# Performance work log

Measured on AMD Instinct MI355X. Metric: run time of the kernel, lower is better.

The kernel has to match this reference:

```python
import jax, jax.numpy as jnp
import numpy as np

B, X, C = 8, 256, 256  # batch, feature axis, topfreq

def setup_inputs() -> dict:
    key = jax.random.key(0)
    k1, k2, k3, k4 = jax.random.split(key, 4)
    return {
        "amplitude": jax.random.normal(k1, (B, X, C), dtype=jnp.float32),
        "phase": jax.random.normal(k2, (B, X, C), dtype=jnp.float32),
        "A": jax.random.normal(k3, (C, C), dtype=jnp.float32),
        "w_amplitude": jnp.asarray(0.5, dtype=jnp.float32),
        "w_phase": jnp.asarray(0.5, dtype=jnp.float32),
        # uniform noise for gumbel sampling; keep away from 0 to avoid -log(-log(0))
        "gumbel_u": jax.random.uniform(k4, (B, C, C, 2), dtype=jnp.float32, minval=1e-6, maxval=1.0),
    }

def reference(amplitude, phase, A, w_amplitude, w_phase, gumbel_u):
    # pairwise diffs: (b, x, c, c)
    a_diff = amplitude[..., :, None] - amplitude[..., None, :]
    p_diff = phase[..., :, None] - phase[..., None, :]
    fused = w_amplitude * a_diff + w_phase * p_diff
    # einsum 'dd,bxcd->bxcd' == multiply by diag(A) along last dim
    temp = jnp.diagonal(A) * fused
    # einsum 'bxcd,bxcd->bcd' == sum of squares over x
    dist = jnp.sum(temp * temp, axis=1)  # (b, c, c)
    exp_dist = 1.0 / (dist + 1e-10)
    eye = jnp.eye(C, dtype=exp_dist.dtype)
    off_diag = 1.0 - eye
    exp_dist = exp_dist * off_diag
    exp_max = jax.lax.stop_gradient(jnp.max(exp_dist, axis=-1, keepdims=True))
    p = exp_dist / exp_max
    p = (p * off_diag + eye) * 0.99  # (b, c, c) in (0, 0.99]
    # bernoulli via 2-class gumbel-softmax (tau=1, hard, straight-through)
    logit = jnp.log(p / (1.0 - p))
    logits = jnp.stack([logit, -logit], axis=-1)  # (b, c, c, 2)
    g = -jnp.log(-jnp.log(gumbel_u))
    y = jax.nn.softmax(logits + g, axis=-1)
    y0 = y[..., 0]
    hard0 = (y0 > y[..., 1]).astype(y.dtype)
    sample = hard0 - jax.lax.stop_gradient(y0) + y0  # straight-through
    mask = sample.mean(axis=0)  # (c, c)
    return mask
```

## Files before the change

### kernel.cpp

```cpp
#include <hip/hip_runtime.h>

#define BB 8
#define XX 256
#define CC 256
#define TC 4
#define G  8


#define STEPU(UC, ACC) {                         \
    float diff = __fsub_rn(UC, ud);              \
    float t    = __fmul_rn(dAd, diff);           \
    float sq   = __fmul_rn(t, t);                \
    ACC = __fadd_rn(ACC, sq);                    \
}

#define LOADG(BA, BP, GIDX) {                    \
    const float* _a = ampbd + (size_t)(GIDX) * G * CC; \
    const float* _p = phbd  + (size_t)(GIDX) * G * CC; \
    _Pragma("unroll")                            \
    for (int i = 0; i < G; ++i) {                \
        BA[i] = _a[(size_t)i * CC];              \
        BP[i] = _p[(size_t)i * CC];              \
    }                                            \
}

#define COMPG(BA, BP, GIDX) {                    \
    const int _xb = (GIDX) * G;                  \
    _Pragma("unroll")                            \
    for (int i = 0; i < G; ++i) {                \
        const float av = BA[i];                  \
        const float pv = BP[i];                  \
        const float ud = __fadd_rn(__fmul_rn(wa, av), __fmul_rn(wp, pv)); \
        const float4 uc = cols[_xb + i];         \
        STEPU(uc.x, acc0)                        \
        STEPU(uc.y, acc1)                        \
        STEPU(uc.z, acc2)                        \
        STEPU(uc.w, acc3)                        \
    }                                            \
}

template<int XPB>
__device__ __forceinline__ void dist_loop(
    const float* __restrict__ ampbd, const float* __restrict__ phbd,
    const float4* cols, float wa, float wp, float dAd,
    float& acc0, float& acc1, float& acc2, float& acc3)
{
    constexpr int NG = XPB / G;
    float b0A[G], b0P[G], b1A[G], b1P[G];
    LOADG(b0A, b0P, 0)
    for (int g = 0; g + 2 < NG; g += 2) {
        LOADG(b1A, b1P, g + 1)
        COMPG(b0A, b0P, g)
        LOADG(b0A, b0P, g + 2)
        COMPG(b1A, b1P, g + 1)
    }
    LOADG(b1A, b1P, NG - 1)
    COMPG(b0A, b0P, NG - 2)
    COMPG(b1A, b1P, NG - 1)
}

template<int XPB>
__device__ __forceinline__ void stage_cols(
    const float* __restrict__ amp, const float* __restrict__ ph,
    int b, int x0, int c0, float wa, float wp, float4* cols)
{
    if (threadIdx.x < XPB) {
        const int x = threadIdx.x;
        const size_t base = ((size_t)b * XX + (x0 + x)) * CC + c0;
        const float4 a4 = *(const float4*)(amp + base);
        const float4 p4 = *(const float4*)(ph  + base);
        float4 u;
        u.x = __fadd_rn(__fmul_rn(wa, a4.x), __fmul_rn(wp, p4.x));
        u.y = __fadd_rn(__fmul_rn(wa, a4.y), __fmul_rn(wp, p4.y));
        u.z = __fadd_rn(__fmul_rn(wa, a4.z), __fmul_rn(wp, p4.z));
        u.w = __fadd_rn(__fmul_rn(wa, a4.w), __fmul_rn(wp, p4.w));
        cols[x] = u;
    }
    __syncthreads();
}

__device__ __forceinline__ void epilogue(
    float dist0, float dist1, float dist2, float dist3,
    int b, int c0, int d, const float* __restrict__ gu,
    float* __restrict__ out, float (*wmax)[4])
{
    float ed[TC];
    ed[0] = (d == c0)     ? 0.0f : __fdiv_rn(1.0f, __fadd_rn(dist0, 1e-10f));
    ed[1] = (d == c0 + 1) ? 0.0f : __fdiv_rn(1.0f, __fadd_rn(dist1, 1e-10f));
    ed[2] = (d == c0 + 2) ? 0.0f : __fdiv_rn(1.0f, __fadd_rn(dist2, 1e-10f));
    ed[3] = (d == c0 + 3) ? 0.0f : __fdiv_rn(1.0f, __fadd_rn(dist3, 1e-10f));

    const int wave = threadIdx.x >> 6;
    const int lane = threadIdx.x & 63;
#pragma unroll
    for (int j = 0; j < TC; ++j) {
        float v = ed[j];
#pragma unroll
        for (int m = 1; m < 64; m <<= 1) v = fmaxf(v, __shfl_xor(v, m));
        if (lane == 0) wmax[j][wave] = v;
    }
    __syncthreads();

#pragma unroll
    for (int j = 0; j < TC; ++j) {
        const int c = c0 + j;
        float em = fmaxf(fmaxf(wmax[j][0], wmax[j][1]), fmaxf(wmax[j][2], wmax[j][3]));
        float p;
        if (d == c) {
            p = 0.99f;
        } else {
            p = __fmul_rn(__fdiv_rn(ed[j], em), 0.99f);
        }
        float logit = logf(__fdiv_rn(p, __fsub_rn(1.0f, p)));

        const float2 g2 = *(const float2*)(gu + (((size_t)b * CC + c) * CC + d) * 2);
        float g0 = -logf(-logf(g2.x));
        float g1 = -logf(-logf(g2.y));

        float a0 = __fadd_rn(logit, g0);
        float a1 = __fadd_rn(-logit, g1);
        float m  = fmaxf(a0, a1);
        float e0 = expf(__fsub_rn(a0, m));
        float e1 = expf(__fsub_rn(a1, m));
        float s  = __fadd_rn(e0, e1);
        float y0 = __fdiv_rn(e0, s);
        float y1 = __fdiv_rn(e1, s);
        if (y0 > y1) {
            atomicAdd(&out[(size_t)c * CC + d], 0.125f);
        }
    }
}


__global__ __launch_bounds__(256, 4) void k_dist(
    const float* __restrict__ amp, const float* __restrict__ ph,
    const float* __restrict__ A,   const float* __restrict__ wAp,
    const float* __restrict__ wPp, float* __restrict__ wsd)
{
    const int d    = threadIdx.x;
    const int c0   = blockIdx.x * TC;
    const int b    = blockIdx.y;
    const int half = blockIdx.z;
    const int x0   = half * (XX / 2);

    const float wa = wAp[0];
    const float wp = wPp[0];

    __shared__ float4 cols[XX / 2];
    stage_cols<XX / 2>(amp, ph, b, x0, c0, wa, wp, cols);

    const float dAd = A[(size_t)d * CC + d];
    const float* ampbd = amp + ((size_t)b * XX + x0) * CC + d;
    const float* phbd  = ph  + ((size_t)b * XX + x0) * CC + d;

    float acc0 = 0.0f, acc1 = 0.0f, acc2 = 0.0f, acc3 = 0.0f;
    dist_loop<XX / 2>(ampbd, phbd, cols, wa, wp, dAd, acc0, acc1, acc2, acc3);

    float* w = wsd + (((size_t)half * BB + b) * CC + c0) * CC + d;
    w[0 * CC] = acc0;
    w[1 * CC] = acc1;
    w[2 * CC] = acc2;
    w[3 * CC] = acc3;
}

__global__ __launch_bounds__(256, 2) void k_epi(
    const float* __restrict__ wsd, const float* __restrict__ gu,
    float* __restrict__ out)
{
    const int d  = threadIdx.x;
    const int c0 = blockIdx.x * TC;
    const int b  = blockIdx.y;

    const float* w0 = wsd + (((size_t)0 * BB + b) * CC + c0) * CC + d;
    const float* w1 = wsd + (((size_t)1 * BB + b) * CC + c0) * CC + d;
    float dist0 = __fadd_rn(w0[0 * CC], w1[0 * CC]);
    float dist1 = __fadd_rn(w0[1 * CC], w1[1 * CC]);
    float dist2 = __fadd_rn(w0[2 * CC], w1[2 * CC]);
    float dist3 = __fadd_rn(w0[3 * CC], w1[3 * CC]);

    __shared__ float wmax[TC][4];
    epilogue(dist0, dist1, dist2, dist3, b, c0, d, gu, out, wmax);
}


__global__ __launch_bounds__(256, 2) void k_fused(
    const float* __restrict__ amp, const float* __restrict__ ph,
    const float* __restrict__ A,   const float* __restrict__ wAp,
    const float* __restrict__ wPp, const float* __restrict__ gu,
    float* __restrict__ out)
{
    const int d  = threadIdx.x;
    const int c0 = blockIdx.x * TC;
    const int b  = blockIdx.y;

    const float wa = wAp[0];
    const float wp = wPp[0];

    __shared__ float4 cols[XX];
    stage_cols<XX>(amp, ph, b, 0, c0, wa, wp, cols);

    const float dAd = A[(size_t)d * CC + d];
    const float* ampbd = amp + (size_t)b * XX * CC + d;
    const float* phbd  = ph  + (size_t)b * XX * CC + d;

    float acc0 = 0.0f, acc1 = 0.0f, acc2 = 0.0f, acc3 = 0.0f;
    dist_loop<XX>(ampbd, phbd, cols, wa, wp, dAd, acc0, acc1, acc2, acc3);

    __shared__ float wmax[TC][4];
    epilogue(acc0, acc1, acc2, acc3, b, c0, d, gu, out, wmax);
}

extern "C" void kernel_launch(void* const* d_in, const int* in_sizes, int n_in,
                              void* d_out, int out_size, void* d_ws, size_t ws_size,
                              hipStream_t stream) {
    const float* amp = (const float*)d_in[0];
    const float* ph  = (const float*)d_in[1];
    const float* A   = (const float*)d_in[2];
    const float* wa  = (const float*)d_in[3];
    const float* wp  = (const float*)d_in[4];
    const float* gu  = (const float*)d_in[5];
    float* out = (float*)d_out;

    hipMemsetAsync(out, 0, (size_t)CC * CC * sizeof(float), stream);

    const size_t need = 2ull * BB * CC * CC * sizeof(float);
    if (ws_size >= need) {
        float* wsd = (float*)d_ws;
        dim3 g1(CC / TC, BB, 2);
        k_dist<<<g1, 256, 0, stream>>>(amp, ph, A, wa, wp, wsd);
        dim3 g2(CC / TC, BB);
        k_epi<<<g2, 256, 0, stream>>>(wsd, gu, out);
    } else {
        dim3 g(CC / TC, BB);
        k_fused<<<g, 256, 0, stream>>>(amp, ph, A, wa, wp, gu, out);
    }
}
```

Before: 92.00 us.

## Precompute fused u and expand squared distance as norms minus dot products

Adds a pre-pass kernel that computes u = wa*amp + wp*ph once into workspace, so the distance kernel reads one array instead of two. The per-x squared difference is rewritten as |u_c|^2 + |u_d|^2 - 2 u_c·u_d, accumulated with FMAs, and the diag(A)^2 scale is moved into the epilogue. The x reduction is split four ways instead of two, and the distance kernel's occupancy bound is raised. The expansion risks cancellation error when u_c and u_d are close, which could flip Bernoulli samples relative to the reference, and it adds a kernel launch plus extra workspace traffic.

```diff
diff --git a/kernel.cpp b/kernel.cpp
--- a/kernel.cpp
+++ b/kernel.cpp
@@ -5,6 +5,169 @@
 #define CC 256
 #define TC 4
 #define G  8
+#define SPLIT 4
+#define XH (XX / SPLIT)
+
+
+
+__device__ __forceinline__ void epilogue(
+    float dist0, float dist1, float dist2, float dist3,
+    int b, int c0, int d, const float* __restrict__ gu,
+    float* __restrict__ out, float (*wmax)[4])
+{
+    float ed[TC];
+    ed[0] = (d == c0)     ? 0.0f : __fdiv_rn(1.0f, __fadd_rn(dist0, 1e-10f));
+    ed[1] = (d == c0 + 1) ? 0.0f : __fdiv_rn(1.0f, __fadd_rn(dist1, 1e-10f));
+    ed[2] = (d == c0 + 2) ? 0.0f : __fdiv_rn(1.0f, __fadd_rn(dist2, 1e-10f));
+    ed[3] = (d == c0 + 3) ? 0.0f : __fdiv_rn(1.0f, __fadd_rn(dist3, 1e-10f));
+
+    const int wave = threadIdx.x >> 6;
+    const int lane = threadIdx.x & 63;
+#pragma unroll
+    for (int j = 0; j < TC; ++j) {
+        float v = ed[j];
+#pragma unroll
+        for (int m = 1; m < 64; m <<= 1) v = fmaxf(v, __shfl_xor(v, m));
+        if (lane == 0) wmax[j][wave] = v;
+    }
+    __syncthreads();
+
+#pragma unroll
+    for (int j = 0; j < TC; ++j) {
+        const int c = c0 + j;
+        float em = fmaxf(fmaxf(wmax[j][0], wmax[j][1]), fmaxf(wmax[j][2], wmax[j][3]));
+        float p;
+        if (d == c) {
+            p = 0.99f;
+        } else {
+            p = __fmul_rn(__fdiv_rn(ed[j], em), 0.99f);
+        }
+        float logit = logf(__fdiv_rn(p, __fsub_rn(1.0f, p)));
+
+        const float2 g2 = *(const float2*)(gu + (((size_t)b * CC + c) * CC + d) * 2);
+        float g0 = -logf(-logf(g2.x));
+        float g1 = -logf(-logf(g2.y));
+
+        float a0 = __fadd_rn(logit, g0);
+        float a1 = __fadd_rn(-logit, g1);
+        float m  = fmaxf(a0, a1);
+        float e0 = expf(__fsub_rn(a0, m));
+        float e1 = expf(__fsub_rn(a1, m));
+        float s  = __fadd_rn(e0, e1);
+        float y0 = __fdiv_rn(e0, s);
+        float y1 = __fdiv_rn(e1, s);
+        if (y0 > y1) {
+            atomicAdd(&out[(size_t)c * CC + d], 0.125f);
+        }
+    }
+}
+
+
+__global__ __launch_bounds__(256) void k_u(
+    const float* __restrict__ amp, const float* __restrict__ ph,
+    const float* __restrict__ wAp, const float* __restrict__ wPp,
+    float* __restrict__ u)
+{
+    const float wa = wAp[0], wp = wPp[0];
+    const int i = blockIdx.x * 256 + threadIdx.x;
+    const float4 a = ((const float4*)amp)[i];
+    const float4 p = ((const float4*)ph)[i];
+    float4 r;
+    r.x = __fadd_rn(__fmul_rn(wa, a.x), __fmul_rn(wp, p.x));
+    r.y = __fadd_rn(__fmul_rn(wa, a.y), __fmul_rn(wp, p.y));
+    r.z = __fadd_rn(__fmul_rn(wa, a.z), __fmul_rn(wp, p.z));
+    r.w = __fadd_rn(__fmul_rn(wa, a.w), __fmul_rn(wp, p.w));
+    ((float4*)u)[i] = r;
+}
+
+#define ULOAD(BU, GIDX) {                                  \
+    const float* _p = ud_ptr + (size_t)(GIDX) * G * CC;    \
+    _Pragma("unroll")                                      \
+    for (int i = 0; i < G; ++i) BU[i] = _p[(size_t)i * CC]; }
+
+#define UCOMP(BU, GIDX) {                                  \
+    const int _xb = (GIDX) * G;                            \
+    _Pragma("unroll")                                      \
+    for (int i = 0; i < G; ++i) {                          \
+        const float udv = BU[i];                           \
+        const float4 c4 = colsU[_xb + i];                  \
+        gacc0 = fmaf(c4.x, udv, gacc0);                    \
+        gacc1 = fmaf(c4.y, udv, gacc1);                    \
+        gacc2 = fmaf(c4.z, udv, gacc2);                    \
+        gacc3 = fmaf(c4.w, udv, gacc3);                    \
+        sacc  = fmaf(udv, udv, sacc);                      \
+    } }
+
+__global__ __launch_bounds__(256, 8) void k_dist(
+    const float* __restrict__ u,
+    float* __restrict__ wsd)
+{
+    const int d    = threadIdx.x;
+    const int c0   = blockIdx.x * TC;
+    const int b    = blockIdx.y;
+    const int x0   = blockIdx.z * XH;
+
+    __shared__ float4 colsU[XH];
+    if (threadIdx.x < XH) {
+        colsU[threadIdx.x] =
+            *(const float4*)(u + ((size_t)b * XX + x0 + threadIdx.x) * CC + c0);
+    }
+    __syncthreads();
+
+    const float* ud_ptr = u + ((size_t)b * XX + x0) * CC + d;
+
+    float gacc0 = 0.0f, gacc1 = 0.0f, gacc2 = 0.0f, gacc3 = 0.0f, sacc = 0.0f;
+
+    constexpr int NGH = XH / G;
+    float b0[G], b1[G];
+    ULOAD(b0, 0)
+    for (int g = 0; g + 2 < NGH; g += 2) {
+        ULOAD(b1, g + 1)
+        UCOMP(b0, g)
+        ULOAD(b0, g + 2)
+        UCOMP(b1, g + 1)
+    }
+    ULOAD(b1, NGH - 1)
+    UCOMP(b0, NGH - 2)
+    UCOMP(b1, NGH - 1)
+
+    __shared__ float sS[CC];
+    sS[d] = sacc;
+    __syncthreads();
+    const float sc0 = sS[c0], sc1 = sS[c0 + 1], sc2 = sS[c0 + 2], sc3 = sS[c0 + 3];
+
+    float* w = wsd + (((size_t)blockIdx.z * BB + b) * CC + c0) * CC + d;
+    w[0 * CC] = fmaf(-2.0f, gacc0, __fadd_rn(sc0, sacc));
+    w[1 * CC] = fmaf(-2.0f, gacc1, __fadd_rn(sc1, sacc));
+    w[2 * CC] = fmaf(-2.0f, gacc2, __fadd_rn(sc2, sacc));
+    w[3 * CC] = fmaf(-2.0f, gacc3, __fadd_rn(sc3, sacc));
+}
+
+__global__ __launch_bounds__(256, 2) void k_epi(
+    const float* __restrict__ wsd, const float* __restrict__ A,
+    const float* __restrict__ gu,  float* __restrict__ out)
+{
+    const int d  = threadIdx.x;
+    const int c0 = blockIdx.x * TC;
+    const int b  = blockIdx.y;
+
+    const float dAd  = A[(size_t)d * CC + d];
+    const float dAd2 = __fmul_rn(dAd, dAd);
+
+    float dist[TC];
+#pragma unroll
+    for (int j = 0; j < TC; ++j) {
+        const size_t ro = ((size_t)b * CC + c0 + j) * CC + d;
+        float p = wsd[ro];
+#pragma unroll
+        for (int h = 1; h < SPLIT; ++h)
+            p = __fadd_rn(p, wsd[(size_t)h * BB * CC * CC + ro]);
+        dist[j] = __fmul_rn(dAd2, p);
+    }
+
+    __shared__ float wmax[TC][4];
+    epilogue(dist[0], dist[1], dist[2], dist[3], b, c0, d, gu, out, wmax);
+}
 
 
 #define STEPU(UC, ACC) {                         \
@@ -39,150 +202,6 @@
     }                                            \
 }
 
-template<int XPB>
-__device__ __forceinline__ void dist_loop(
-    const float* __restrict__ ampbd, const float* __restrict__ phbd,
-    const float4* cols, float wa, float wp, float dAd,
-    float& acc0, float& acc1, float& acc2, float& acc3)
-{
-    constexpr int NG = XPB / G;
-    float b0A[G], b0P[G], b1A[G], b1P[G];
-    LOADG(b0A, b0P, 0)
-    for (int g = 0; g + 2 < NG; g += 2) {
-        LOADG(b1A, b1P, g + 1)
-        COMPG(b0A, b0P, g)
-        LOADG(b0A, b0P, g + 2)
-        COMPG(b1A, b1P, g + 1)
-    }
-    LOADG(b1A, b1P, NG - 1)
-    COMPG(b0A, b0P, NG - 2)
-    COMPG(b1A, b1P, NG - 1)
-}
-
-template<int XPB>
-__device__ __forceinline__ void stage_cols(
-    const float* __restrict__ amp, const float* __restrict__ ph,
-    int b, int x0, int c0, float wa, float wp, float4* cols)
-{
-    if (threadIdx.x < XPB) {
-        const int x = threadIdx.x;
-        const size_t base = ((size_t)b * XX + (x0 + x)) * CC + c0;
-        const float4 a4 = *(const float4*)(amp + base);
-        const float4 p4 = *(const float4*)(ph  + base);
-        float4 u;
-        u.x = __fadd_rn(__fmul_rn(wa, a4.x), __fmul_rn(wp, p4.x));
-        u.y = __fadd_rn(__fmul_rn(wa, a4.y), __fmul_rn(wp, p4.y));
-        u.z = __fadd_rn(__fmul_rn(wa, a4.z), __fmul_rn(wp, p4.z));
-        u.w = __fadd_rn(__fmul_rn(wa, a4.w), __fmul_rn(wp, p4.w));
-        cols[x] = u;
-    }
-    __syncthreads();
-}
-
-__device__ __forceinline__ void epilogue(
-    float dist0, float dist1, float dist2, float dist3,
-    int b, int c0, int d, const float* __restrict__ gu,
-    float* __restrict__ out, float (*wmax)[4])
-{
-    float ed[TC];
-    ed[0] = (d == c0)     ? 0.0f : __fdiv_rn(1.0f, __fadd_rn(dist0, 1e-10f));
-    ed[1] = (d == c0 + 1) ? 0.0f : __fdiv_rn(1.0f, __fadd_rn(dist1, 1e-10f));
-    ed[2] = (d == c0 + 2) ? 0.0f : __fdiv_rn(1.0f, __fadd_rn(dist2, 1e-10f));
-    ed[3] = (d == c0 + 3) ? 0.0f : __fdiv_rn(1.0f, __fadd_rn(dist3, 1e-10f));
-
-    const int wave = threadIdx.x >> 6;
-    const int lane = threadIdx.x & 63;
-#pragma unroll
-    for (int j = 0; j < TC; ++j) {
-        float v = ed[j];
-#pragma unroll
-        for (int m = 1; m < 64; m <<= 1) v = fmaxf(v, __shfl_xor(v, m));
-        if (lane == 0) wmax[j][wave] = v;
-    }
-    __syncthreads();
-
-#pragma unroll
-    for (int j = 0; j < TC; ++j) {
-        const int c = c0 + j;
-        float em = fmaxf(fmaxf(wmax[j][0], wmax[j][1]), fmaxf(wmax[j][2], wmax[j][3]));
-        float p;
-        if (d == c) {
-            p = 0.99f;
-        } else {
-            p = __fmul_rn(__fdiv_rn(ed[j], em), 0.99f);
-        }
-        float logit = logf(__fdiv_rn(p, __fsub_rn(1.0f, p)));
-
-        const float2 g2 = *(const float2*)(gu + (((size_t)b * CC + c) * CC + d) * 2);
-        float g0 = -logf(-logf(g2.x));
-        float g1 = -logf(-logf(g2.y));
-
-        float a0 = __fadd_rn(logit, g0);
-        float a1 = __fadd_rn(-logit, g1);
-        float m  = fmaxf(a0, a1);
-        float e0 = expf(__fsub_rn(a0, m));
-        float e1 = expf(__fsub_rn(a1, m));
-        float s  = __fadd_rn(e0, e1);
-        float y0 = __fdiv_rn(e0, s);
-        float y1 = __fdiv_rn(e1, s);
-        if (y0 > y1) {
-            atomicAdd(&out[(size_t)c * CC + d], 0.125f);
-        }
-    }
-}
-
-
-__global__ __launch_bounds__(256, 4) void k_dist(
-    const float* __restrict__ amp, const float* __restrict__ ph,
-    const float* __restrict__ A,   const float* __restrict__ wAp,
-    const float* __restrict__ wPp, float* __restrict__ wsd)
-{
-    const int d    = threadIdx.x;
-    const int c0   = blockIdx.x * TC;
-    const int b    = blockIdx.y;
-    const int half = blockIdx.z;
-    const int x0   = half * (XX / 2);
-
-    const float wa = wAp[0];
-    const float wp = wPp[0];
-
-    __shared__ float4 cols[XX / 2];
-    stage_cols<XX / 2>(amp, ph, b, x0, c0, wa, wp, cols);
-
-    const float dAd = A[(size_t)d * CC + d];
-    const float* ampbd = amp + ((size_t)b * XX + x0) * CC + d;
-    const float* phbd  = ph  + ((size_t)b * XX + x0) * CC + d;
-
-    float acc0 = 0.0f, acc1 = 0.0f, acc2 = 0.0f, acc3 = 0.0f;
-    dist_loop<XX / 2>(ampbd, phbd, cols, wa, wp, dAd, acc0, acc1, acc2, acc3);
-
-    float* w = wsd + (((size_t)half * BB + b) * CC + c0) * CC + d;
-    w[0 * CC] = acc0;
-    w[1 * CC] = acc1;
-    w[2 * CC] = acc2;
-    w[3 * CC] = acc3;
-}
-
-__global__ __launch_bounds__(256, 2) void k_epi(
-    const float* __restrict__ wsd, const float* __restrict__ gu,
-    float* __restrict__ out)
-{
-    const int d  = threadIdx.x;
-    const int c0 = blockIdx.x * TC;
-    const int b  = blockIdx.y;
-
-    const float* w0 = wsd + (((size_t)0 * BB + b) * CC + c0) * CC + d;
-    const float* w1 = wsd + (((size_t)1 * BB + b) * CC + c0) * CC + d;
-    float dist0 = __fadd_rn(w0[0 * CC], w1[0 * CC]);
-    float dist1 = __fadd_rn(w0[1 * CC], w1[1 * CC]);
-    float dist2 = __fadd_rn(w0[2 * CC], w1[2 * CC]);
-    float dist3 = __fadd_rn(w0[3 * CC], w1[3 * CC]);
-
-    __shared__ float wmax[TC][4];
-    epilogue(dist0, dist1, dist2, dist3, b, c0, d, gu, out, wmax);
-}
-
-
 __global__ __launch_bounds__(256, 2) void k_fused(
     const float* __restrict__ amp, const float* __restrict__ ph,
     const float* __restrict__ A,   const float* __restrict__ wAp,
@@ -197,14 +216,39 @@
     const float wp = wPp[0];
 
     __shared__ float4 cols[XX];
-    stage_cols<XX>(amp, ph, b, 0, c0, wa, wp, cols);
+    {
+        const int x = threadIdx.x;
+        const size_t base = ((size_t)b * XX + x) * CC + c0;
+        const float4 a4 = *(const float4*)(amp + base);
+        const float4 p4 = *(const float4*)(ph  + base);
+        float4 uu;
+        uu.x = __fadd_rn(__fmul_rn(wa, a4.x), __fmul_rn(wp, p4.x));
+        uu.y = __fadd_rn(__fmul_rn(wa, a4.y), __fmul_rn(wp, p4.y));
+        uu.z = __fadd_rn(__fmul_rn(wa, a4.z), __fmul_rn(wp, p4.z));
+        uu.w = __fadd_rn(__fmul_rn(wa, a4.w), __fmul_rn(wp, p4.w));
+        cols[x] = uu;
+    }
+    __syncthreads();
 
     const float dAd = A[(size_t)d * CC + d];
     const float* ampbd = amp + (size_t)b * XX * CC + d;
     const float* phbd  = ph  + (size_t)b * XX * CC + d;
 
     float acc0 = 0.0f, acc1 = 0.0f, acc2 = 0.0f, acc3 = 0.0f;
-    dist_loop<XX>(ampbd, phbd, cols, wa, wp, dAd, acc0, acc1, acc2, acc3);
+    constexpr int NG = XX / G;
+    {
+        float b0A[G], b0P[G], b1A[G], b1P[G];
+        LOADG(b0A, b0P, 0)
+        for (int g = 0; g + 2 < NG; g += 2) {
+            LOADG(b1A, b1P, g + 1)
+            COMPG(b0A, b0P, g)
+            LOADG(b0A, b0P, g + 2)
+            COMPG(b1A, b1P, g + 1)
+        }
+        LOADG(b1A, b1P, NG - 1)
+        COMPG(b0A, b0P, NG - 2)
+        COMPG(b1A, b1P, NG - 1)
+    }
 
     __shared__ float wmax[TC][4];
     epilogue(acc0, acc1, acc2, acc3, b, c0, d, gu, out, wmax);
@@ -223,13 +267,17 @@
 
     hipMemsetAsync(out, 0, (size_t)CC * CC * sizeof(float), stream);
 
-    const size_t need = 2ull * BB * CC * CC * sizeof(float);
+    const size_t uElems = (size_t)BB * XX * CC;
+    const size_t pElems = (size_t)SPLIT * BB * CC * CC;
+    const size_t need = (uElems + pElems) * sizeof(float);
     if (ws_size >= need) {
-        float* wsd = (float*)d_ws;
-        dim3 g1(CC / TC, BB, 2);
-        k_dist<<<g1, 256, 0, stream>>>(amp, ph, A, wa, wp, wsd);
+        float* ud  = (float*)d_ws;
+        float* wsd = ud + uElems;
+        k_u<<<uElems / 4 / 256, 256, 0, stream>>>(amp, ph, wa, wp, ud);
+        dim3 g1(CC / TC, BB, SPLIT);
+        k_dist<<<g1, 256, 0, stream>>>(ud, wsd);
         dim3 g2(CC / TC, BB);
-        k_epi<<<g2, 256, 0, stream>>>(wsd, gu, out);
+        k_epi<<<g2, 256, 0, stream>>>(wsd, A, gu, out);
     } else {
         dim3 g(CC / TC, BB);
         k_fused<<<g, 256, 0, stream>>>(amp, ph, A, wa, wp, gu, out);
```

New measurement: 85.47 us. 1.08x faster.
